# Performance work log

Measured on AMD Instinct MI355X. Metric: run time of the kernel, lower is better.

Reference implementation:

```python
import jax, jax.numpy as jnp
import numpy as np

N = 50000
E = 1600000
IN = 128
HID = 128
OUT = 64
NL = 200000
NEG_SLOPE = 0.2


def _glorot(key, shape):
    fan_in, fan_out = shape[0], shape[-1]
    s = jnp.sqrt(6.0 / (fan_in + fan_out))
    return jax.random.uniform(key, shape, jnp.float32, -s, s)


def setup_inputs() -> dict:
    key = jax.random.key(0)
    ks = jax.random.split(key, 16)
    x = jax.random.normal(ks[0], (N, IN), jnp.float32)
    edge_index = jax.random.randint(ks[1], (2, E), 0, N, dtype=jnp.int32)
    edge_label_index = jax.random.randint(ks[2], (2, NL), 0, N, dtype=jnp.int32)
    return {
        "x": x,
        "edge_index": edge_index,
        "edge_label_index": edge_label_index,
        "W1": _glorot(ks[3], (IN, HID)),  "a1s": _glorot(ks[4], (HID,)),  "a1d": _glorot(ks[5], (HID,)),  "b1": jnp.zeros((HID,), jnp.float32),
        "W2": _glorot(ks[6], (HID, HID)), "a2s": _glorot(ks[7], (HID,)),  "a2d": _glorot(ks[8], (HID,)),  "b2": jnp.zeros((HID,), jnp.float32),
        "W3": _glorot(ks[9], (HID, HID)), "a3s": _glorot(ks[10], (HID,)), "a3d": _glorot(ks[11], (HID,)), "b3": jnp.zeros((HID,), jnp.float32),
        "W4": _glorot(ks[12], (HID, OUT)), "b4": jnp.zeros((OUT,), jnp.float32),
    }


def _add_self_loops(edge_index, n):
    loop = jnp.arange(n, dtype=edge_index.dtype)
    return jnp.concatenate([edge_index, jnp.stack([loop, loop])], axis=1)


def gat_conv(x, edge_index, W, a_s, a_d, b):
    """PyG GATConv, heads=1, add_self_loops=True: gather, LeakyReLU score,
    segment softmax over destination nodes, scatter-add aggregate."""
    n = x.shape[0]
    ei = _add_self_loops(edge_index, n)
    src, dst = ei[0], ei[1]
    h = x @ W                                    # [N, H]
    e = jax.nn.leaky_relu((h @ a_s)[src] + (h @ a_d)[dst], NEG_SLOPE)  # [E']
    m = jax.ops.segment_max(e, dst, num_segments=n)
    p = jnp.exp(e - m[dst])
    s = jax.ops.segment_sum(p, dst, num_segments=n)
    alpha = p / s[dst]                           # segment softmax
    out = jax.ops.segment_sum(h[src] * alpha[:, None], dst, num_segments=n)
    return out + b


def gcn_conv(x, edge_index, W, b):
    """PyG GCNConv: self-loops + symmetric degree normalization."""
    n = x.shape[0]
    ei = _add_self_loops(edge_index, n)
    src, dst = ei[0], ei[1]
    h = x @ W
    deg = jax.ops.segment_sum(jnp.ones(src.shape, h.dtype), dst, num_segments=n)
    dinv = jax.lax.rsqrt(deg)
    norm = dinv[src] * dinv[dst]                 # [E']
    out = jax.ops.segment_sum(h[src] * norm[:, None], dst, num_segments=n)
    return out + b


def reference(x, edge_index, edge_label_index,
              W1, a1s, a1d, b1, W2, a2s, a2d, b2,
              W3, a3s, a3d, b3, W4, b4):
    h = jax.nn.relu(gat_conv(x, edge_index, W1, a1s, a1d, b1))
    h = jax.nn.relu(gat_conv(h, edge_index, W2, a2s, a2d, b2))
    h = jax.nn.relu(gat_conv(h, edge_index, W3, a3s, a3d, b3))
    z = gcn_conv(h, edge_index, W4, b4)          # [N, OUT]
    # decode: dot product of endpoint embeddings -> link logits [NL]
    return (z[edge_label_index[0]] * z[edge_label_index[1]]).sum(axis=-1)
```

## Files before the change

kernel.cpp:

```cpp
#include <hip/hip_runtime.h>
#include <hip/hip_fp16.h>
#include <math.h>

#define NN   50000
#define NE   1600000
#define NLBL 200000
#define CAP  80
#define NEG  0.2f
#define NBK  196
#define CAPB 8800
#define CHK  4096
#define GBIN 391

typedef unsigned short u16;
typedef _Float16 half8 __attribute__((ext_vector_type(8)));
typedef float floatx4 __attribute__((ext_vector_type(4)));


__device__ void ph_bin(int blk, const int* __restrict__ ei,
                       int* __restrict__ gcnt, unsigned* __restrict__ bins) {
    __shared__ int cntL[NBK];
    __shared__ int offL[NBK];
    __shared__ int curL[NBK];
    __shared__ int curG[NBK];
    __shared__ unsigned stage[CHK];
    const int tid = threadIdx.x;
    const int e0 = blk * CHK + tid * 16;
    const bool act = (e0 + 15) < NE;

    unsigned pk[16];
    int bb[16];
    if (act) {
#pragma unroll
        for (int g = 0; g < 4; ++g) {
            int4 s4 = *(const int4*)&ei[e0 + g * 4];
            int4 d4 = *(const int4*)&ei[NE + e0 + g * 4];
            int sa[4] = {s4.x, s4.y, s4.z, s4.w};
            int da[4] = {d4.x, d4.y, d4.z, d4.w};
#pragma unroll
            for (int k = 0; k < 4; ++k) {
                int idx = g * 4 + k;
                bb[idx] = da[k] >> 8;
                pk[idx] = (unsigned)sa[k] | ((unsigned)(da[k] & 255) << 16)
                        | ((unsigned)bb[idx] << 24);
            }
        }
    }
    for (int i = tid; i < NBK; i += 256) cntL[i] = 0;
    __syncthreads();
    if (act) {
#pragma unroll
        for (int k = 0; k < 16; ++k) atomicAdd(&cntL[bb[k]], 1);
    }
    __syncthreads();
    if (tid < NBK) {
        int acc = 0;
        for (int i = 0; i < tid; ++i) acc += cntL[i];
        offL[tid] = acc;
        curL[tid] = acc;
    }
    __syncthreads();
    for (int i = tid; i < NBK; i += 256) curG[i] = atomicAdd(&gcnt[i], cntL[i]);
    __syncthreads();
    if (act) {
#pragma unroll
        for (int k = 0; k < 16; ++k) {
            int pos = atomicAdd(&curL[bb[k]], 1);
            stage[pos] = pk[k];
        }
    }
    __syncthreads();
    const int tot = offL[NBK - 1] + cntL[NBK - 1];
    for (int j = tid; j < tot; j += 256) {
        unsigned v = stage[j];
        int b = v >> 24;
        int lr = j - offL[b];
        bins[(size_t)b * CAPB + curG[b] + lr] = v & 0x00FFFFFFu;
    }
}

__global__ __launch_bounds__(256) void k_build(const unsigned* __restrict__ bins,
                                               const int* __restrict__ gcnt,
                                               int* __restrict__ cnt,
                                               u16* __restrict__ csr) {
    __shared__ u16 rows[256 * CAP];
    __shared__ int cur[256];
    const int b = blockIdx.x, tid = threadIdx.x;
    const int d0 = b << 8;
    const int nd = min(256, NN - d0);
    if (tid < nd) { cur[tid] = 1; rows[tid * CAP] = (u16)(d0 + tid); }
    __syncthreads();
    const int n = gcnt[b];
    for (int i = tid; i < n; i += 256) {
        unsigned v = bins[(size_t)b * CAPB + i];
        int s = v & 0xFFFF, dl = (v >> 16) & 0xFF;
        int pos = atomicAdd(&cur[dl], 1);
        if (pos < CAP) rows[dl * CAP + pos] = (u16)s;
    }
    __syncthreads();
    const unsigned* rw = (const unsigned*)rows;
    unsigned* cw = (unsigned*)(csr + (size_t)d0 * CAP);
    const int tot = nd * (CAP / 2);
    for (int i = tid; i < tot; i += 256) cw[i] = rw[i];
    if (tid < nd) cnt[d0 + tid] = cur[tid];
}


__global__ __launch_bounds__(256) void k_pre(const float* __restrict__ W1f,
                                             const float* __restrict__ W2f,
                                             const float* __restrict__ W3f,
                                             const float* __restrict__ W4f,
                                             half8* __restrict__ Wf1,
                                             half8* __restrict__ Wf2,
                                             half8* __restrict__ Wf3,
                                             half8* __restrict__ Wf4,
                                             int* __restrict__ gcnt) {
    if (blockIdx.x == 28) {
        int i = threadIdx.x;
        if (i < NBK) gcnt[i] = 0;
        return;
    }
    int e = blockIdx.x * 256 + threadIdx.x;
    const float* W;
    half8* Wf;
    int nout, le;
    if (e < 2048)      { W = W1f; Wf = Wf1; nout = 128; le = e; }
    else if (e < 4096) { W = W2f; Wf = Wf2; nout = 128; le = e - 2048; }
    else if (e < 6144) { W = W3f; Wf = Wf3; nout = 128; le = e - 4096; }
    else               { W = W4f; Wf = Wf4; nout = 64;  le = e - 6144; }
    int c = le >> 8, rem = le & 255, ks = rem >> 6, lane = rem & 63;
    int n = lane & 15, quad = lane >> 4;
    int col = c * 16 + n, k0 = ks * 32 + quad * 8;
    half8 v;
#pragma unroll
    for (int j = 0; j < 8; ++j) v[j] = (_Float16)W[(size_t)(k0 + j) * nout + col];
    Wf[le] = v;
}


template <int NOUT, bool ATTN, typename TA>
__device__ __forceinline__ void gemm_tile(int gt, int lane,
                                          const TA* __restrict__ A,
                                          const half8* __restrict__ Wf,
                                          __half* __restrict__ C,
                                          const float* __restrict__ a_s,
                                          const float* __restrict__ a_d,
                                          float* __restrict__ asv,
                                          float* __restrict__ adv) {
    constexpr int CT = NOUT / 16;
    constexpr int OSTR = (NOUT == 64) ? 64 : 128;
    const int n = lane & 15, quad = lane >> 4;
    if (gt * 16 >= NN) return;
    const int row = gt * 16 + n;

    half8 a[4];
#pragma unroll
    for (int ks = 0; ks < 4; ++ks) {
        int c128 = ks * 32 + quad * 8;
        if constexpr (sizeof(TA) == 2) {
            a[ks] = *(const half8*)((const _Float16*)A + (size_t)row * 128 + c128);
        } else {
            const float* Ap = (const float*)A + (size_t)row * 128 + c128;
            float4 f0 = *(const float4*)Ap;
            float4 f1 = *(const float4*)(Ap + 4);
            half8 v;
            v[0] = (_Float16)f0.x; v[1] = (_Float16)f0.y; v[2] = (_Float16)f0.z; v[3] = (_Float16)f0.w;
            v[4] = (_Float16)f1.x; v[5] = (_Float16)f1.y; v[6] = (_Float16)f1.z; v[7] = (_Float16)f1.w;
            a[ks] = v;
        }
    }

    floatx4 acc[CT];
#pragma unroll
    for (int c = 0; c < CT; ++c) acc[c] = (floatx4){0.f, 0.f, 0.f, 0.f};
#pragma unroll
    for (int c = 0; c < CT; ++c) {
#pragma unroll
        for (int ks = 0; ks < 4; ++ks) {
            half8 b = Wf[(c * 4 + ks) * 64 + lane];
            acc[c] = __builtin_amdgcn_mfma_f32_16x16x32_f16(b, a[ks], acc[c], 0, 0, 0);
        }
    }

#pragma unroll
    for (int c = 0; c < CT; ++c) {
        __half2 h0 = __floats2half2_rn(acc[c][0], acc[c][1]);
        __half2 h1 = __floats2half2_rn(acc[c][2], acc[c][3]);
        uint2 u;
        __builtin_memcpy(&u.x, &h0, 4);
        __builtin_memcpy(&u.y, &h1, 4);
        *(uint2*)&C[(size_t)row * OSTR + c * 16 + quad * 4] = u;
    }

    if (ATTN) {
        float ps = 0.f, pd = 0.f;
#pragma unroll
        for (int c = 0; c < CT; ++c) {
#pragma unroll
            for (int reg = 0; reg < 4; ++reg) {
                float w = acc[c][reg];
                ps = fmaf(w, a_s[c * 16 + quad * 4 + reg], ps);
                pd = fmaf(w, a_d[c * 16 + quad * 4 + reg], pd);
            }
        }
        ps += __shfl_xor(ps, 16); ps += __shfl_xor(ps, 32);
        pd += __shfl_xor(pd, 16); pd += __shfl_xor(pd, 32);
        if (quad == 0) { asv[row] = ps; adv[row] = pd; }
    }
}

__global__ __launch_bounds__(256) void k_bin_gemm1(const int* __restrict__ ei,
                                                   int* __restrict__ gcnt,
                                                   unsigned* __restrict__ bins,
                                                   const float* __restrict__ x,
                                                   const half8* __restrict__ Wf1,
                                                   __half* __restrict__ G,
                                                   const float* __restrict__ a_s,
                                                   const float* __restrict__ a_d,
                                                   float* __restrict__ asv,
                                                   float* __restrict__ adv) {
    if (blockIdx.x < GBIN) { ph_bin(blockIdx.x, ei, gcnt, bins); return; }
    int gt = (blockIdx.x - GBIN) * 4 + (threadIdx.x >> 6);
    gemm_tile<128, true, float>(gt, threadIdx.x & 63, x, Wf1, G, a_s, a_d, asv, adv);
}

template <int NOUT, bool ATTN>
__global__ __launch_bounds__(64) void k_gemm64(const __half* __restrict__ A,
                                               const half8* __restrict__ Wf,
                                               __half* __restrict__ C,
                                               const float* __restrict__ a_s,
                                               const float* __restrict__ a_d,
                                               float* __restrict__ asv,
                                               float* __restrict__ adv) {
    gemm_tile<NOUT, ATTN, __half>(blockIdx.x, threadIdx.x & 63, A, Wf, C,
                                  a_s, a_d, asv, adv);
}

__device__ __forceinline__ void fma_h8v(half8 h, float al, float* acc) {
#pragma unroll
    for (int k = 0; k < 8; ++k) acc[k] = fmaf(al, (float)h[k], acc[k]);
}


__global__ __launch_bounds__(256) void k_gat_agg(const __half* __restrict__ h,
                                                 const int* __restrict__ cnt,
                                                 const u16* __restrict__ csr,
                                                 const float* __restrict__ asv,
                                                 const float* __restrict__ adv,
                                                 const float* __restrict__ bias,
                                                 __half* __restrict__ out) {
    __shared__ float2 metaL[4][88];
    int lane = threadIdx.x & 63, wv = threadIdx.x >> 6;
    int d = blockIdx.x * 4 + wv;
    if (d >= NN) return;
    int deg = cnt[d]; if (deg > CAP) deg = CAP;
    const float advd = adv[d];
    const u16* rowp = csr + (size_t)d * CAP;

    int j0 = lane, j1 = lane + 64;
    int s0 = 0, s1 = 0;
    float e0 = -INFINITY, e1 = -INFINITY;
    if (j0 < deg) {
        s0 = rowp[j0];
        float t = asv[s0] + advd;
        e0 = (t >= 0.f) ? t : NEG * t;
    }
    if (j1 < deg) {
        s1 = rowp[j1];
        float t = asv[s1] + advd;
        e1 = (t >= 0.f) ? t : NEG * t;
    }
    float m = fmaxf(e0, e1);
#pragma unroll
    for (int off = 32; off; off >>= 1) m = fmaxf(m, __shfl_xor(m, off));
    float p0 = (j0 < deg) ? __expf(e0 - m) : 0.f;
    float p1 = (j1 < deg) ? __expf(e1 - m) : 0.f;
    float s = p0 + p1;
#pragma unroll
    for (int off = 32; off; off >>= 1) s += __shfl_xor(s, off);
    float inv = 1.f / s;
    metaL[wv][j0] = make_float2(p0 * inv, __int_as_float(s0));
    if (j1 < 88) metaL[wv][j1] = make_float2(p1 * inv, __int_as_float(s1));

    int slot = lane >> 4, r = lane & 15;
    float acc[8];
#pragma unroll
    for (int k = 0; k < 8; ++k) acc[k] = 0.f;
    int degp = (deg + 3) & ~3;
    for (int base = 0; base < degp; base += 4) {
        float2 ms = metaL[wv][base + slot];
        float al = ms.x;
        int   sj = __float_as_int(ms.y);
        half8 hv = *(const half8*)&h[(size_t)sj * 128 + r * 8];
        fma_h8v(hv, al, acc);
    }
#pragma unroll
    for (int k = 0; k < 8; ++k) {
        acc[k] += __shfl_xor(acc[k], 16);
        acc[k] += __shfl_xor(acc[k], 32);
    }
    if (slot == 0) {
        __half2 ho[4];
#pragma unroll
        for (int k = 0; k < 4; ++k) {
            float oa = fmaxf(acc[2 * k]     + bias[r * 8 + 2 * k],     0.f);
            float ob = fmaxf(acc[2 * k + 1] + bias[r * 8 + 2 * k + 1], 0.f);
            ho[k] = __floats2half2_rn(oa, ob);
        }
        uint4 u;
        __builtin_memcpy(&u, &ho[0], 16);
        *(uint4*)&out[(size_t)d * 128 + r * 8] = u;
    }
}


__global__ __launch_bounds__(256) void k_gcn_agg(const __half* __restrict__ h,
                                                 const int* __restrict__ cnt,
                                                 const u16* __restrict__ csr,
                                                 const float* __restrict__ bias,
                                                 __half* __restrict__ z) {
    __shared__ float2 metaL[4][88];
    int lane = threadIdx.x & 63, wv = threadIdx.x >> 6;
    int d = blockIdx.x * 4 + wv;
    if (d >= NN) return;
    int degc = cnt[d];
    int deg = degc > CAP ? CAP : degc;
    float did = rsqrtf((float)degc);
    const u16* rowp = csr + (size_t)d * CAP;

    int j0 = lane, j1 = lane + 64;
    int s0 = 0, s1 = 0;
    float n0 = 0.f, n1 = 0.f;
    if (j0 < deg) { s0 = rowp[j0]; n0 = rsqrtf((float)cnt[s0]) * did; }
    if (j1 < deg) { s1 = rowp[j1]; n1 = rsqrtf((float)cnt[s1]) * did; }
    metaL[wv][j0] = make_float2(n0, __int_as_float(s0));
    if (j1 < 88) metaL[wv][j1] = make_float2(n1, __int_as_float(s1));

    int slot = lane >> 3, r = lane & 7;
    float acc[8];
#pragma unroll
    for (int k = 0; k < 8; ++k) acc[k] = 0.f;

    int degp = (deg + 7) & ~7;
    for (int base = 0; base < degp; base += 8) {
        float2 ms = metaL[wv][base + slot];
        float nm = ms.x;
        int   sj = __float_as_int(ms.y);
        half8 hv = *(const half8*)&h[(size_t)sj * 64 + r * 8];
        fma_h8v(hv, nm, acc);
    }
#pragma unroll
    for (int k = 0; k < 8; ++k) {
        acc[k] += __shfl_xor(acc[k], 8);
        acc[k] += __shfl_xor(acc[k], 16);
        acc[k] += __shfl_xor(acc[k], 32);
    }
    if (slot == 0) {
        __half2 ho[4];
#pragma unroll
        for (int k = 0; k < 4; ++k) {
            float oa = acc[2 * k]     + bias[r * 8 + 2 * k];
            float ob = acc[2 * k + 1] + bias[r * 8 + 2 * k + 1];
            ho[k] = __floats2half2_rn(oa, ob);
        }
        uint4 u;
        __builtin_memcpy(&u, &ho[0], 16);
        *(uint4*)&z[(size_t)d * 64 + r * 8] = u;
    }
}


__global__ __launch_bounds__(256) void k_decode(const __half* __restrict__ z,
                                                const int* __restrict__ eli,
                                                float* __restrict__ outp) {
    int lane = threadIdx.x & 63, wv = threadIdx.x >> 6;
    int g = lane >> 4, r = lane & 15;
    int idx = (blockIdx.x * 4 + wv) * 4 + g;
    if (idx >= NLBL) return;
    int a = eli[idx], b = eli[NLBL + idx];
    uint2 ua = *(const uint2*)&z[(size_t)a * 64 + r * 4];
    uint2 ub = *(const uint2*)&z[(size_t)b * 64 + r * 4];
    float2 a0 = __half22float2(*(__half2*)&ua.x);
    float2 a1 = __half22float2(*(__half2*)&ua.y);
    float2 b0 = __half22float2(*(__half2*)&ub.x);
    float2 b1 = __half22float2(*(__half2*)&ub.y);
    float v = a0.x * b0.x + a0.y * b0.y + a1.x * b1.x + a1.y * b1.y;
#pragma unroll
    for (int off = 8; off; off >>= 1) v += __shfl_xor(v, off);
    if (r == 0) outp[idx] = v;
}


extern "C" void kernel_launch(void* const* d_in, const int* in_sizes, int n_in,
                              void* d_out, int out_size, void* d_ws, size_t ws_size,
                              hipStream_t stream) {
    const float* x   = (const float*)d_in[0];
    const int*   ei  = (const int*)d_in[1];
    const int*   eli = (const int*)d_in[2];
    const float* W1 = (const float*)d_in[3];
    const float* a1s = (const float*)d_in[4];
    const float* a1d = (const float*)d_in[5];
    const float* b1 = (const float*)d_in[6];
    const float* W2 = (const float*)d_in[7];
    const float* a2s = (const float*)d_in[8];
    const float* a2d = (const float*)d_in[9];
    const float* b2 = (const float*)d_in[10];
    const float* W3 = (const float*)d_in[11];
    const float* a3s = (const float*)d_in[12];
    const float* a3d = (const float*)d_in[13];
    const float* b3 = (const float*)d_in[14];
    const float* W4 = (const float*)d_in[15];
    const float* b4 = (const float*)d_in[16];
    float* outp = (float*)d_out;

    char* p = (char*)d_ws;
    auto alloc = [&](size_t bytes) -> char* {
        char* r = p;
        p += (bytes + 255) & ~(size_t)255;
        return r;
    };
    int*    cnt  = (int*)alloc((size_t)NN * 4);
    u16*    csr  = (u16*)alloc((size_t)NN * CAP * 2);
    int*    gcnt = (int*)alloc((size_t)NBK * 4);
    float*  asv  = (float*)alloc((size_t)NN * 4);
    float*  advv = (float*)alloc((size_t)NN * 4);
    __half* G    = (__half*)alloc((size_t)NN * 128 * 2);
    __half* B1   = (__half*)alloc((size_t)NN * 128 * 2);
    __half* B2   = (__half*)alloc((size_t)NN * 128 * 2);
    __half* zf   = (__half*)alloc((size_t)NN * 64 * 2);
    half8*  Wf1  = (half8*)alloc(2048 * 16);
    half8*  Wf2  = (half8*)alloc(2048 * 16);
    half8*  Wf3  = (half8*)alloc(2048 * 16);
    half8*  Wf4  = (half8*)alloc(1024 * 16);
    unsigned* bins = (unsigned*)alloc((size_t)NBK * CAPB * 4);
    __half* H64  = B2;

    const int gG1   = GBIN + 782;
    const int gGemm = (NN + 15) / 16;
    const int gNode = (NN + 3) / 4;
    const int gDec  = (NLBL + 15) / 16;

    k_pre<<<29, 256, 0, stream>>>(W1, W2, W3, W4, Wf1, Wf2, Wf3, Wf4, gcnt);
    k_bin_gemm1<<<gG1, 256, 0, stream>>>(ei, gcnt, bins, x, Wf1, G, a1s, a1d, asv, advv);
    k_build<<<NBK, 256, 0, stream>>>(bins, gcnt, cnt, csr);

    k_gat_agg<<<gNode, 256, 0, stream>>>(G, cnt, csr, asv, advv, b1, B1);

    k_gemm64<128, true><<<gGemm, 64, 0, stream>>>(B1, Wf2, G, a2s, a2d, asv, advv);
    k_gat_agg<<<gNode, 256, 0, stream>>>(G, cnt, csr, asv, advv, b2, B2);

    k_gemm64<128, true><<<gGemm, 64, 0, stream>>>(B2, Wf3, G, a3s, a3d, asv, advv);
    k_gat_agg<<<gNode, 256, 0, stream>>>(G, cnt, csr, asv, advv, b3, B1);

    k_gemm64<64, false><<<gGemm, 64, 0, stream>>>(B1, Wf4, H64, nullptr, nullptr, nullptr, nullptr);
    k_gcn_agg<<<gNode, 256, 0, stream>>>(H64, cnt, csr, b4, zf);

    k_decode<<<gDec, 256, 0, stream>>>(zf, eli, outp);
}
```

Before: 370.2 us.

## Store GEMM outputs in 32-column planes and split aggregation by feature slice

```diff
diff --git a/kernel.cpp b/kernel.cpp
--- a/kernel.cpp
+++ b/kernel.cpp
@@ -148,7 +148,6 @@
                                           float* __restrict__ asv,
                                           float* __restrict__ adv) {
     constexpr int CT = NOUT / 16;
-    constexpr int OSTR = (NOUT == 64) ? 64 : 128;
     const int n = lane & 15, quad = lane >> 4;
     if (gt * 16 >= NN) return;
     const int row = gt * 16 + n;
@@ -189,7 +188,9 @@
         uint2 u;
         __builtin_memcpy(&u.x, &h0, 4);
         __builtin_memcpy(&u.y, &h1, 4);
-        *(uint2*)&C[(size_t)row * OSTR + c * 16 + quad * 4] = u;
+        int col = c * 16 + quad * 4;
+        int pl = col >> 5, off = col & 31;
+        *(uint2*)&C[((size_t)pl * NN + row) * 32 + off] = u;
     }
 
     if (ATTN) {
@@ -236,38 +237,26 @@
                                   a_s, a_d, asv, adv);
 }
 
-__device__ __forceinline__ void fma_h8v(half8 h, float al, float* acc) {
-#pragma unroll
-    for (int k = 0; k < 8; ++k) acc[k] = fmaf(al, (float)h[k], acc[k]);
-}
-
-
-__global__ __launch_bounds__(256) void k_gat_agg(const __half* __restrict__ h,
-                                                 const int* __restrict__ cnt,
-                                                 const u16* __restrict__ csr,
-                                                 const float* __restrict__ asv,
-                                                 const float* __restrict__ adv,
-                                                 const float* __restrict__ bias,
-                                                 __half* __restrict__ out) {
-    __shared__ float2 metaL[4][88];
+
+__global__ __launch_bounds__(256) void k_scores(const int* __restrict__ cnt,
+                                                const u16* __restrict__ csr,
+                                                const float* __restrict__ asv,
+                                                const float* __restrict__ adv,
+                                                float2* __restrict__ msv) {
     int lane = threadIdx.x & 63, wv = threadIdx.x >> 6;
     int d = blockIdx.x * 4 + wv;
     if (d >= NN) return;
     int deg = cnt[d]; if (deg > CAP) deg = CAP;
     const float advd = adv[d];
     const u16* rowp = csr + (size_t)d * CAP;
-
     int j0 = lane, j1 = lane + 64;
-    int s0 = 0, s1 = 0;
     float e0 = -INFINITY, e1 = -INFINITY;
     if (j0 < deg) {
-        s0 = rowp[j0];
-        float t = asv[s0] + advd;
+        float t = asv[rowp[j0]] + advd;
         e0 = (t >= 0.f) ? t : NEG * t;
     }
     if (j1 < deg) {
-        s1 = rowp[j1];
-        float t = asv[s1] + advd;
+        float t = asv[rowp[j1]] + advd;
         e1 = (t >= 0.f) ? t : NEG * t;
     }
     float m = fmaxf(e0, e1);
@@ -278,51 +267,93 @@
     float s = p0 + p1;
 #pragma unroll
     for (int off = 32; off; off >>= 1) s += __shfl_xor(s, off);
-    float inv = 1.f / s;
-    metaL[wv][j0] = make_float2(p0 * inv, __int_as_float(s0));
-    if (j1 < 88) metaL[wv][j1] = make_float2(p1 * inv, __int_as_float(s1));
-
-    int slot = lane >> 4, r = lane & 15;
+    if (lane == 0) msv[d] = make_float2(m, 1.f / s);
+}
+
+__device__ __forceinline__ void fma_h8v(half8 h, float al, float* acc) {
+#pragma unroll
+    for (int k = 0; k < 8; ++k) acc[k] = fmaf(al, (float)h[k], acc[k]);
+}
+
+
+__global__ __launch_bounds__(256) void k_gat_agg_sl(const __half* __restrict__ h,
+                                                    const int* __restrict__ cnt,
+                                                    const u16* __restrict__ csr,
+                                                    const float* __restrict__ asv,
+                                                    const float* __restrict__ adv,
+                                                    const float2* __restrict__ msv,
+                                                    const float* __restrict__ bias,
+                                                    __half* __restrict__ out) {
+    __shared__ float2 metaL[4][88];
+    int lane = threadIdx.x & 63, wv = threadIdx.x >> 6;
+    int sl = blockIdx.x & 3;
+    int d = (blockIdx.x >> 2) * 4 + wv;
+    int deg = cnt[d]; if (deg > CAP) deg = CAP;
+    const float advd = adv[d];
+    const float2 mi = msv[d];
+    const u16* rowp = csr + (size_t)d * CAP;
+
+    int j0 = lane, j1 = lane + 64;
+    int s0 = 0, s1 = 0;
+    float a0 = 0.f, a1 = 0.f;
+    if (j0 < deg) {
+        s0 = rowp[j0];
+        float t = asv[s0] + advd;
+        float e = (t >= 0.f) ? t : NEG * t;
+        a0 = __expf(e - mi.x) * mi.y;
+    }
+    if (j1 < deg) {
+        s1 = rowp[j1];
+        float t = asv[s1] + advd;
+        float e = (t >= 0.f) ? t : NEG * t;
+        a1 = __expf(e - mi.x) * mi.y;
+    }
+    metaL[wv][j0] = make_float2(a0, __int_as_float(s0));
+    if (j1 < 88) metaL[wv][j1] = make_float2(a1, __int_as_float(s1));
+
+    int slot = lane >> 2, r = lane & 3;
+    const _Float16* hb = (const _Float16*)h + (size_t)sl * NN * 32 + r * 8;
     float acc[8];
 #pragma unroll
     for (int k = 0; k < 8; ++k) acc[k] = 0.f;
-    int degp = (deg + 3) & ~3;
-    for (int base = 0; base < degp; base += 4) {
+    int degp = (deg + 15) & ~15;
+    for (int base = 0; base < degp; base += 16) {
         float2 ms = metaL[wv][base + slot];
-        float al = ms.x;
-        int   sj = __float_as_int(ms.y);
-        half8 hv = *(const half8*)&h[(size_t)sj * 128 + r * 8];
-        fma_h8v(hv, al, acc);
+        half8 hv = *(const half8*)(hb + (size_t)__float_as_int(ms.y) * 32);
+        fma_h8v(hv, ms.x, acc);
     }
 #pragma unroll
     for (int k = 0; k < 8; ++k) {
+        acc[k] += __shfl_xor(acc[k], 4);
+        acc[k] += __shfl_xor(acc[k], 8);
         acc[k] += __shfl_xor(acc[k], 16);
         acc[k] += __shfl_xor(acc[k], 32);
     }
     if (slot == 0) {
+        int cb = sl * 32 + r * 8;
         __half2 ho[4];
 #pragma unroll
         for (int k = 0; k < 4; ++k) {
-            float oa = fmaxf(acc[2 * k]     + bias[r * 8 + 2 * k],     0.f);
-            float ob = fmaxf(acc[2 * k + 1] + bias[r * 8 + 2 * k + 1], 0.f);
+            float oa = fmaxf(acc[2 * k]     + bias[cb + 2 * k],     0.f);
+            float ob = fmaxf(acc[2 * k + 1] + bias[cb + 2 * k + 1], 0.f);
             ho[k] = __floats2half2_rn(oa, ob);
         }
         uint4 u;
         __builtin_memcpy(&u, &ho[0], 16);
-        *(uint4*)&out[(size_t)d * 128 + r * 8] = u;
-    }
-}
-
-
-__global__ __launch_bounds__(256) void k_gcn_agg(const __half* __restrict__ h,
-                                                 const int* __restrict__ cnt,
-                                                 const u16* __restrict__ csr,
-                                                 const float* __restrict__ bias,
-                                                 __half* __restrict__ z) {
+        *(uint4*)&out[(size_t)d * 128 + cb] = u;
+    }
+}
+
+
+__global__ __launch_bounds__(256) void k_gcn_agg_sl(const __half* __restrict__ h,
+                                                    const int* __restrict__ cnt,
+                                                    const u16* __restrict__ csr,
+                                                    const float* __restrict__ bias,
+                                                    __half* __restrict__ z) {
     __shared__ float2 metaL[4][88];
     int lane = threadIdx.x & 63, wv = threadIdx.x >> 6;
-    int d = blockIdx.x * 4 + wv;
-    if (d >= NN) return;
+    int sl = blockIdx.x & 1;
+    int d = (blockIdx.x >> 1) * 4 + wv;
     int degc = cnt[d];
     int deg = degc > CAP ? CAP : degc;
     float did = rsqrtf((float)degc);
@@ -336,36 +367,36 @@
     metaL[wv][j0] = make_float2(n0, __int_as_float(s0));
     if (j1 < 88) metaL[wv][j1] = make_float2(n1, __int_as_float(s1));
 
-    int slot = lane >> 3, r = lane & 7;
+    int slot = lane >> 2, r = lane & 3;
+    const _Float16* hb = (const _Float16*)h + (size_t)sl * NN * 32 + r * 8;
     float acc[8];
 #pragma unroll
     for (int k = 0; k < 8; ++k) acc[k] = 0.f;
-
-    int degp = (deg + 7) & ~7;
-    for (int base = 0; base < degp; base += 8) {
+    int degp = (deg + 15) & ~15;
+    for (int base = 0; base < degp; base += 16) {
         float2 ms = metaL[wv][base + slot];
-        float nm = ms.x;
-        int   sj = __float_as_int(ms.y);
-        half8 hv = *(const half8*)&h[(size_t)sj * 64 + r * 8];
-        fma_h8v(hv, nm, acc);
+        half8 hv = *(const half8*)(hb + (size_t)__float_as_int(ms.y) * 32);
+        fma_h8v(hv, ms.x, acc);
     }
 #pragma unroll
     for (int k = 0; k < 8; ++k) {
+        acc[k] += __shfl_xor(acc[k], 4);
         acc[k] += __shfl_xor(acc[k], 8);
         acc[k] += __shfl_xor(acc[k], 16);
         acc[k] += __shfl_xor(acc[k], 32);
     }
     if (slot == 0) {
+        int cb = sl * 32 + r * 8;
         __half2 ho[4];
 #pragma unroll
         for (int k = 0; k < 4; ++k) {
-            float oa = acc[2 * k]     + bias[r * 8 + 2 * k];
-            float ob = acc[2 * k + 1] + bias[r * 8 + 2 * k + 1];
+            float oa = acc[2 * k]     + bias[cb + 2 * k];
+            float ob = acc[2 * k + 1] + bias[cb + 2 * k + 1];
             ho[k] = __floats2half2_rn(oa, ob);
         }
         uint4 u;
         __builtin_memcpy(&u, &ho[0], 16);
-        *(uint4*)&z[(size_t)d * 64 + r * 8] = u;
+        *(uint4*)&z[(size_t)d * 64 + cb] = u;
     }
 }
 
@@ -422,38 +453,44 @@
     int*    cnt  = (int*)alloc((size_t)NN * 4);
     u16*    csr  = (u16*)alloc((size_t)NN * CAP * 2);
     int*    gcnt = (int*)alloc((size_t)NBK * 4);
-    float*  asv  = (float*)alloc((size_t)NN * 4);
-    float*  advv = (float*)alloc((size_t)NN * 4);
+    float*  asvA = (float*)alloc((size_t)NN * 4);
+    float*  advA = (float*)alloc((size_t)NN * 4);
+    float*  asvB = (float*)alloc((size_t)NN * 4);
+    float*  advB = (float*)alloc((size_t)NN * 4);
+    float2* msv  = (float2*)alloc((size_t)NN * 8);
     __half* G    = (__half*)alloc((size_t)NN * 128 * 2);
-    __half* B1   = (__half*)alloc((size_t)NN * 128 * 2);
-    __half* B2   = (__half*)alloc((size_t)NN * 128 * 2);
+    __half* B    = (__half*)alloc((size_t)NN * 128 * 2);
     __half* zf   = (__half*)alloc((size_t)NN * 64 * 2);
     half8*  Wf1  = (half8*)alloc(2048 * 16);
     half8*  Wf2  = (half8*)alloc(2048 * 16);
     half8*  Wf3  = (half8*)alloc(2048 * 16);
     half8*  Wf4  = (half8*)alloc(1024 * 16);
     unsigned* bins = (unsigned*)alloc((size_t)NBK * CAPB * 4);
-    __half* H64  = B2;
 
     const int gG1   = GBIN + 782;
     const int gGemm = (NN + 15) / 16;
-    const int gNode = (NN + 3) / 4;
+    const int gSc   = (NN + 3) / 4;
+    const int gAgg  = gSc * 4;
+    const int gGcn  = gSc * 2;
     const int gDec  = (NLBL + 15) / 16;
 
     k_pre<<<29, 256, 0, stream>>>(W1, W2, W3, W4, Wf1, Wf2, Wf3, Wf4, gcnt);
-    k_bin_gemm1<<<gG1, 256, 0, stream>>>(ei, gcnt, bins, x, Wf1, G, a1s, a1d, asv, advv);
+    k_bin_gemm1<<<gG1, 256, 0, stream>>>(ei, gcnt, bins, x, Wf1, G, a1s, a1d, asvA, advA);
     k_build<<<NBK, 256, 0, stream>>>(bins, gcnt, cnt, csr);
 
-    k_gat_agg<<<gNode, 256, 0, stream>>>(G, cnt, csr, asv, advv, b1, B1);
-
-    k_gemm64<128, true><<<gGemm, 64, 0, stream>>>(B1, Wf2, G, a2s, a2d, asv, advv);
-    k_gat_agg<<<gNode, 256, 0, stream>>>(G, cnt, csr, asv, advv, b2, B2);
-
-    k_gemm64<128, true><<<gGemm, 64, 0, stream>>>(B2, Wf3, G, a3s, a3d, asv, advv);
-    k_gat_agg<<<gNode, 256, 0, stream>>>(G, cnt, csr, asv, advv, b3, B1);
-
-    k_gemm64<64, false><<<gGemm, 64, 0, stream>>>(B1, Wf4, H64, nullptr, nullptr, nullptr, nullptr);
-    k_gcn_agg<<<gNode, 256, 0, stream>>>(H64, cnt, csr, b4, zf);
+    k_scores<<<gSc, 256, 0, stream>>>(cnt, csr, asvA, advA, msv);
+    k_gat_agg_sl<<<gAgg, 256, 0, stream>>>(G, cnt, csr, asvA, advA, msv, b1, B);
+    k_gemm64<128, true><<<gGemm, 64, 0, stream>>>(B, Wf2, G, a2s, a2d, asvB, advB);
+
+    k_scores<<<gSc, 256, 0, stream>>>(cnt, csr, asvB, advB, msv);
+    k_gat_agg_sl<<<gAgg, 256, 0, stream>>>(G, cnt, csr, asvB, advB, msv, b2, B);
+    k_gemm64<128, true><<<gGemm, 64, 0, stream>>>(B, Wf3, G, a3s, a3d, asvA, advA);
+
+    k_scores<<<gSc, 256, 0, stream>>>(cnt, csr, asvA, advA, msv);
+    k_gat_agg_sl<<<gAgg, 256, 0, stream>>>(G, cnt, csr, asvA, advA, msv, b3, B);
+    k_gemm64<64, false><<<gGemm, 64, 0, stream>>>(B, Wf4, G, nullptr, nullptr, nullptr, nullptr);
+
+    k_gcn_agg_sl<<<gGcn, 256, 0, stream>>>(G, cnt, csr, b4, zf);
 
     k_decode<<<gDec, 256, 0, stream>>>(zf, eli, outp);
 }
```

New measurement: 545.4 us. 47.3% more time.
